# Kernel optimization log

Hardware: AMD Instinct MI355X
Metric: run time of the kernel (lower is better)

## Reference

```python
import jax, jax.numpy as jnp
import numpy as np

N_NODES = 100000
N_EDGES = 1600000
N_FEAT = 128
HIDDEN = 128
N_CLASSES = 10
N_GRAPHS = 512


def setup_inputs() -> dict:
    key = jax.random.key(0)
    ks = jax.random.split(key, 20)

    def lin(k, fan_in, fan_out, bias=True):
        kw, kb = jax.random.split(k)
        s = 1.0 / np.sqrt(fan_in)
        W = jax.random.uniform(kw, (fan_in, fan_out), jnp.float32, -s, s)
        if bias:
            b = jax.random.uniform(kb, (fan_out,), jnp.float32, -s, s)
            return W, b
        return W

    x = jax.random.normal(ks[0], (N_NODES, N_FEAT), jnp.float32)
    edge_index = jax.random.randint(ks[1], (2, N_EDGES), 0, N_NODES)
    batch = jnp.sort(jax.random.randint(ks[2], (N_NODES,), 0, N_GRAPHS))

    w1l, b1 = lin(ks[3], N_FEAT, HIDDEN)
    w1r = lin(ks[4], N_FEAT, HIDDEN, bias=False)
    w2l, b2 = lin(ks[5], HIDDEN, HIDDEN)
    w2r = lin(ks[6], HIDDEN, HIDDEN, bias=False)
    w3l, b3 = lin(ks[7], HIDDEN, HIDDEN)
    w3r = lin(ks[8], HIDDEN, HIDDEN, bias=False)
    gate_w, gate_b = lin(ks[9], HIDDEN, 1)
    lin1_w, lin1_b = lin(ks[10], HIDDEN, HIDDEN)
    lin2_w, lin2_b = lin(ks[11], HIDDEN, N_CLASSES)

    return dict(x=x, edge_index=edge_index, batch=batch,
                w1l=w1l, b1=b1, w1r=w1r,
                w2l=w2l, b2=b2, w2r=w2r,
                w3l=w3l, b3=b3, w3r=w3r,
                gate_w=gate_w, gate_b=gate_b,
                lin1_w=lin1_w, lin1_b=lin1_b,
                lin2_w=lin2_w, lin2_b=lin2_b)


def _sage_conv(x, src, dst, Wl, bl, Wr, n_nodes):
    # PyG SAGEConv(mean): out = lin_l(mean_{j in N(i)} x_j) + lin_r(x_i)
    msg_sum = jax.ops.segment_sum(x[src], dst, num_segments=n_nodes)
    cnt = jax.ops.segment_sum(jnp.ones((src.shape[0], 1), x.dtype), dst,
                              num_segments=n_nodes)
    mean = msg_sum / jnp.maximum(cnt, 1.0)
    return mean @ Wl + bl + x @ Wr


def reference(x, edge_index, batch,
              w1l, b1, w1r, w2l, b2, w2r, w3l, b3, w3r,
              gate_w, gate_b, lin1_w, lin1_b, lin2_w, lin2_b):
    n = x.shape[0]
    src, dst = edge_index[0], edge_index[1]

    h = jax.nn.relu(_sage_conv(x, src, dst, w1l, b1, w1r, n))
    h = jax.nn.relu(_sage_conv(h, src, dst, w2l, b2, w2r, n))
    h = jax.nn.relu(_sage_conv(h, src, dst, w3l, b3, w3r, n))

    # AttentionalAggregation: scatter-softmax of gate over graph segments
    gate = h @ gate_w + gate_b                                  # [N, 1]
    m = jax.ops.segment_max(gate, batch, num_segments=N_GRAPHS)  # [G, 1]
    e = jnp.exp(gate - m[batch])
    s = jax.ops.segment_sum(e, batch, num_segments=N_GRAPHS)     # [G, 1]
    alpha = e / s[batch]
    pooled = jax.ops.segment_sum(alpha * h, batch, num_segments=N_GRAPHS)  # [G, H]

    out = jax.nn.relu(pooled @ lin1_w + lin1_b)
    # dropout is identity in eval mode
    out = out @ lin2_w + lin2_b
    return jax.nn.log_softmax(out, axis=-1)
```

## Files before the change

kernel.cpp:

```cpp
#include <hip/hip_runtime.h>
#include <stdint.h>

#define N_NODES 100000
#define N_EDGES 1600000
#define NF 128
#define NG 512
#define NC 10

#define NBUCK ((N_NODES + 255) / 256)
#define EPB 8192

#define BSTRIDE 264

#define CVT_B 6250
#define BT_B 384
#define BOUNDS_B 3

typedef short short8 __attribute__((ext_vector_type(8)));
typedef float f32x4 __attribute__((ext_vector_type(4)));

__device__ __forceinline__ unsigned short f2b(float f) {
    unsigned u = __float_as_uint(f);
    u += 0x7fffu + ((u >> 16) & 1u);
    return (unsigned short)(u >> 16);
}
__device__ __forceinline__ float lo16(unsigned v) { return __uint_as_float(v << 16); }
__device__ __forceinline__ float hi16(unsigned v) { return __uint_as_float(v & 0xffff0000u); }

__global__ __launch_bounds__(256) void bucket_count(const int* __restrict__ dst, int* __restrict__ bcount) {
    __shared__ int h[NBUCK];
    for (int i = threadIdx.x; i < NBUCK; i += 256) h[i] = 0;
    __syncthreads();
    const int base = blockIdx.x * EPB;
    const int lim = min(base + EPB, N_EDGES);
    for (int i = base + threadIdx.x; i < lim; i += 256) atomicAdd(&h[dst[i] >> 8], 1);
    __syncthreads();
    for (int i = threadIdx.x; i < NBUCK; i += 256)
        if (h[i]) atomicAdd(&bcount[i], h[i]);
}

__global__ __launch_bounds__(512) void bucket_scan(const int* __restrict__ bcount, int* __restrict__ bbase,
                                                   int* __restrict__ gcursor, int* __restrict__ rowptr) {
    __shared__ int sh[512];
    const int t = threadIdx.x;
    int v = (t < NBUCK) ? bcount[t] : 0;
    sh[t] = v;
    __syncthreads();
    for (int off = 1; off < 512; off <<= 1) {
        int u = (t >= off) ? sh[t - off] : 0;
        __syncthreads();
        sh[t] += u;
        __syncthreads();
    }
    if (t < NBUCK) {
        int e = sh[t] - v;
        bbase[t] = e;
        gcursor[t] = e;
    }
    if (t == NBUCK - 1) bbase[NBUCK] = sh[t];
    if (t == 0) rowptr[N_NODES] = N_EDGES;
}

__global__ __launch_bounds__(256) void bucket_scatter(const int* __restrict__ src, const int* __restrict__ dst,
                                                      int* __restrict__ gcursor, unsigned* __restrict__ brec) {
    __shared__ int h[NBUCK];
    for (int i = threadIdx.x; i < NBUCK; i += 256) h[i] = 0;
    __syncthreads();
    const int base = blockIdx.x * EPB;
    const int lim = min(base + EPB, N_EDGES);
    for (int i = base + threadIdx.x; i < lim; i += 256) atomicAdd(&h[dst[i] >> 8], 1);
    __syncthreads();
    for (int i = threadIdx.x; i < NBUCK; i += 256) {
        int c = h[i];
        if (c) h[i] = atomicAdd(&gcursor[i], c);
    }
    __syncthreads();
    for (int i = base + threadIdx.x; i < lim; i += 256) {
        int d = dst[i];
        int pos = atomicAdd(&h[d >> 8], 1);
        brec[pos] = ((unsigned)(d & 255) << 17) | (unsigned)src[i];
    }
}

__global__ __launch_bounds__(256) void bucket_fill(const unsigned* __restrict__ brec, const int* __restrict__ bbase,
                                                   int* __restrict__ rowptr, int* __restrict__ eidx) {
    __shared__ int nh[256];
    __shared__ int sc[256];
    const int b = blockIdx.x, t = threadIdx.x;
    const int beg = bbase[b], end = bbase[b + 1];
    nh[t] = 0;
    __syncthreads();
    for (int i = beg + t; i < end; i += 256) atomicAdd(&nh[brec[i] >> 17], 1);
    __syncthreads();
    int cnt = nh[t];
    sc[t] = cnt;
    __syncthreads();
    for (int off = 1; off < 256; off <<= 1) {
        int u = (t >= off) ? sc[t - off] : 0;
        __syncthreads();
        sc[t] += u;
        __syncthreads();
    }
    int excl = sc[t] - cnt;
    int node = b * 256 + t;
    if (node < N_NODES) rowptr[node] = beg + excl;
    nh[t] = beg + excl;
    __syncthreads();
    for (int i = beg + t; i < end; i += 256) {
        unsigned r = brec[i];
        int pos = atomicAdd(&nh[r >> 17], 1);
        eidx[pos] = (int)(r & 0x1FFFFu);
    }
}

__global__ __launch_bounds__(256) void prep_kernel(const float* __restrict__ x, unsigned short* __restrict__ xb,
                                                   const float* __restrict__ w1l, const float* __restrict__ w1r,
                                                   const float* __restrict__ w2l, const float* __restrict__ w2r,
                                                   const float* __restrict__ w3l, const float* __restrict__ w3r,
                                                   unsigned short* __restrict__ Bt,
                                                   const int* __restrict__ batch, int* __restrict__ gstart) {
    const int b = blockIdx.x, t = threadIdx.x;
    if (b < CVT_B) {
        int i = b * 256 + t;
        const float4* ip = (const float4*)x;
        float4 a = ip[2 * i], c = ip[2 * i + 1];
        uint4 o;
        o.x = (unsigned)f2b(a.x) | ((unsigned)f2b(a.y) << 16);
        o.y = (unsigned)f2b(a.z) | ((unsigned)f2b(a.w) << 16);
        o.z = (unsigned)f2b(c.x) | ((unsigned)f2b(c.y) << 16);
        o.w = (unsigned)f2b(c.z) | ((unsigned)f2b(c.w) << 16);
        ((uint4*)xb)[i] = o;
    } else if (b < CVT_B + BT_B) {
        int i = (b - CVT_B) * 256 + t;
        int layer = i / (128 * 256);
        int r = i % (128 * 256);
        int n = r / 256, k = r % 256;
        const float* wl = (layer == 0) ? w1l : (layer == 1) ? w2l : w3l;
        const float* wr = (layer == 0) ? w1r : (layer == 1) ? w2r : w3r;
        float v = (k < 128) ? wl[k * 128 + n] : wr[(k - 128) * 128 + n];
        Bt[i] = f2b(v);
    } else {
        int g = (b - CVT_B - BT_B) * 256 + t;
        if (g > NG) return;
        int lo = 0, hi = N_NODES;
        while (lo < hi) {
            int mid = (lo + hi) >> 1;
            if (batch[mid] < g) lo = mid + 1; else hi = mid;
        }
        gstart[g] = lo;
    }
}

__global__ __launch_bounds__(256) void agg_kernel(const unsigned short* __restrict__ F,
                                                  const int* __restrict__ rowptr,
                                                  const int* __restrict__ eidx,
                                                  unsigned short* __restrict__ M) {
    int node = blockIdx.x * 4 + (threadIdx.x >> 6);
    if (node >= N_NODES) return;
    const int lane = threadIdx.x & 63;
    const int quad = lane >> 4, ql = lane & 15;
    const int beg = rowptr[node], end = rowptr[node + 1];
    const uint4* F4 = (const uint4*)F;

    float a0 = 0.f, a1 = 0.f, a2 = 0.f, a3 = 0.f, a4 = 0.f, a5 = 0.f, a6 = 0.f, a7 = 0.f;
    int t = beg + quad;
    for (; t + 12 < end; t += 16) {
        int r0 = eidx[t];
        int r1 = eidx[t + 4];
        int r2 = eidx[t + 8];
        int r3 = eidx[t + 12];
        uint4 v0 = F4[(size_t)r0 * 16 + ql];
        uint4 v1 = F4[(size_t)r1 * 16 + ql];
        uint4 v2 = F4[(size_t)r2 * 16 + ql];
        uint4 v3 = F4[(size_t)r3 * 16 + ql];
        a0 += lo16(v0.x) + lo16(v1.x) + lo16(v2.x) + lo16(v3.x);
        a1 += hi16(v0.x) + hi16(v1.x) + hi16(v2.x) + hi16(v3.x);
        a2 += lo16(v0.y) + lo16(v1.y) + lo16(v2.y) + lo16(v3.y);
        a3 += hi16(v0.y) + hi16(v1.y) + hi16(v2.y) + hi16(v3.y);
        a4 += lo16(v0.z) + lo16(v1.z) + lo16(v2.z) + lo16(v3.z);
        a5 += hi16(v0.z) + hi16(v1.z) + hi16(v2.z) + hi16(v3.z);
        a6 += lo16(v0.w) + lo16(v1.w) + lo16(v2.w) + lo16(v3.w);
        a7 += hi16(v0.w) + hi16(v1.w) + hi16(v2.w) + hi16(v3.w);
    }
    for (; t < end; t += 4) {
        uint4 v0 = F4[(size_t)eidx[t] * 16 + ql];
        a0 += lo16(v0.x); a1 += hi16(v0.x);
        a2 += lo16(v0.y); a3 += hi16(v0.y);
        a4 += lo16(v0.z); a5 += hi16(v0.z);
        a6 += lo16(v0.w); a7 += hi16(v0.w);
    }
    a0 += __shfl_xor(a0, 16); a0 += __shfl_xor(a0, 32);
    a1 += __shfl_xor(a1, 16); a1 += __shfl_xor(a1, 32);
    a2 += __shfl_xor(a2, 16); a2 += __shfl_xor(a2, 32);
    a3 += __shfl_xor(a3, 16); a3 += __shfl_xor(a3, 32);
    a4 += __shfl_xor(a4, 16); a4 += __shfl_xor(a4, 32);
    a5 += __shfl_xor(a5, 16); a5 += __shfl_xor(a5, 32);
    a6 += __shfl_xor(a6, 16); a6 += __shfl_xor(a6, 32);
    a7 += __shfl_xor(a7, 16); a7 += __shfl_xor(a7, 32);

    if (quad == 0) {
        float inv = 1.0f / (float)max(end - beg, 1);
        uint4 o;
        o.x = (unsigned)f2b(a0 * inv) | ((unsigned)f2b(a1 * inv) << 16);
        o.y = (unsigned)f2b(a2 * inv) | ((unsigned)f2b(a3 * inv) << 16);
        o.z = (unsigned)f2b(a4 * inv) | ((unsigned)f2b(a5 * inv) << 16);
        o.w = (unsigned)f2b(a6 * inv) | ((unsigned)f2b(a7 * inv) << 16);
        ((uint4*)M)[(size_t)node * 16 + ql] = o;
    }
}

__global__ __launch_bounds__(256, 2) void gemm_kernel(const unsigned short* __restrict__ Am,
                                                      const unsigned short* __restrict__ Ax,
                                                      const unsigned short* __restrict__ Bt,
                                                      const float* __restrict__ bias,
                                                      unsigned short* __restrict__ Out,
                                                      const float* __restrict__ gatew,
                                                      const float* __restrict__ gateb,
                                                      float* __restrict__ gate) {
    const int t = threadIdx.x;
    const int wave = t >> 6, lane = t & 63;
    const int lrow = lane & 15, quad = lane >> 4;
    const int row0 = blockIdx.x * 64 + wave * 16;

    __shared__ __attribute__((aligned(16))) unsigned short Bs[128 * BSTRIDE];

#pragma unroll
    for (int i = 0; i < 16; ++i) {
        int u = t + i * 256;
        int r = u >> 5, seg = u & 31;
        *(uint4*)(Bs + r * BSTRIDE + seg * 8) = *(const uint4*)(Bt + r * 256 + seg * 8);
    }
    __syncthreads();

    int arow = row0 + lrow;
    if (arow > N_NODES - 1) arow = N_NODES - 1;

    f32x4 acc[8];
#pragma unroll
    for (int nt = 0; nt < 8; ++nt) acc[nt] = (f32x4){0.f, 0.f, 0.f, 0.f};

#pragma unroll
    for (int c = 0; c < 8; ++c) {
        const unsigned short* Aarr = (c < 4) ? Am : Ax;
        const int kb = (c & 3) * 32 + quad * 8;
        short8 af = *(const short8*)(Aarr + (size_t)arow * 128 + kb);
        const int kf = c * 32 + quad * 8;
#pragma unroll
        for (int nt = 0; nt < 8; ++nt) {
            short8 bf = *(const short8*)(Bs + (nt * 16 + lrow) * BSTRIDE + kf);
            acc[nt] = __builtin_amdgcn_mfma_f32_16x16x32_bf16(af, bf, acc[nt], 0, 0, 0);
        }
    }

    float gpart[4] = {0.f, 0.f, 0.f, 0.f};
#pragma unroll
    for (int nt = 0; nt < 8; ++nt) {
        int col = nt * 16 + lrow;
        float bc = bias[col];
        float gw = gatew ? gatew[col] : 0.f;
#pragma unroll
        for (int r = 0; r < 4; ++r) {
            int row = row0 + quad * 4 + r;
            if (row < N_NODES) {
                float v = fmaxf(acc[nt][r] + bc, 0.f);
                Out[(size_t)row * 128 + col] = f2b(v);
                gpart[r] += v * gw;
            }
        }
    }
    if (gatew) {
#pragma unroll
        for (int r = 0; r < 4; ++r) {
            gpart[r] += __shfl_xor(gpart[r], 1);
            gpart[r] += __shfl_xor(gpart[r], 2);
            gpart[r] += __shfl_xor(gpart[r], 4);
            gpart[r] += __shfl_xor(gpart[r], 8);
        }
        if (lrow == 0) {
            float gb = gateb[0];
#pragma unroll
            for (int r = 0; r < 4; ++r) {
                int row = row0 + quad * 4 + r;
                if (row < N_NODES) gate[row] = gpart[r] + gb;
            }
        }
    }
}

__global__ __launch_bounds__(256) void pool_mlp_kernel(const unsigned short* __restrict__ h,
                                                       const float* __restrict__ gate,
                                                       const int* __restrict__ gstart,
                                                       const float* __restrict__ l1w,
                                                       const float* __restrict__ l1b,
                                                       const float* __restrict__ l2w,
                                                       const float* __restrict__ l2b,
                                                       float* __restrict__ out) {
    int wv = threadIdx.x >> 6;
    int g = blockIdx.x * 4 + wv;
    int lane = threadIdx.x & 63;
    __shared__ float pooled_s[4][128];
    __shared__ float hid_s[4][128];
    if (g >= NG) return;

    int beg = gstart[g], end = gstart[g + 1];

    float m = -INFINITY;
    for (int i = beg + lane; i < end; i += 64) m = fmaxf(m, gate[i]);
#pragma unroll
    for (int o = 32; o; o >>= 1) m = fmaxf(m, __shfl_xor(m, o));
    float s = 0.f;
    for (int i = beg + lane; i < end; i += 64) s += expf(gate[i] - m);
#pragma unroll
    for (int o = 32; o; o >>= 1) s += __shfl_xor(s, o);
    float invs = (s > 0.f) ? 1.0f / s : 0.f;

    float ax = 0.f, ay = 0.f;
    const unsigned* hb = (const unsigned*)h;
    int i = beg;
    for (; i + 2 <= end; i += 2) {
        float w0 = expf(gate[i] - m) * invs;
        float w1 = expf(gate[i + 1] - m) * invs;
        unsigned v0 = hb[(size_t)i * 64 + lane];
        unsigned v1 = hb[(size_t)(i + 1) * 64 + lane];
        ax += w0 * lo16(v0) + w1 * lo16(v1);
        ay += w0 * hi16(v0) + w1 * hi16(v1);
    }
    for (; i < end; ++i) {
        float w = expf(gate[i] - m) * invs;
        unsigned v = hb[(size_t)i * 64 + lane];
        ax += w * lo16(v);
        ay += w * hi16(v);
    }
    pooled_s[wv][2 * lane] = ax;
    pooled_s[wv][2 * lane + 1] = ay;

    float h0 = l1b[lane], h1 = l1b[lane + 64];
    for (int k = 0; k < 128; ++k) {
        float pv = pooled_s[wv][k];
        h0 += pv * l1w[k * 128 + lane];
        h1 += pv * l1w[k * 128 + lane + 64];
    }
    hid_s[wv][lane] = fmaxf(h0, 0.f);
    hid_s[wv][lane + 64] = fmaxf(h1, 0.f);

    float o10 = 0.f;
    if (lane < NC) {
        o10 = l2b[lane];
        for (int k = 0; k < 128; ++k) o10 += hid_s[wv][k] * l2w[k * NC + lane];
    }
    float mm = -INFINITY;
#pragma unroll
    for (int j = 0; j < NC; ++j) mm = fmaxf(mm, __shfl(o10, j));
    float ss = 0.f;
#pragma unroll
    for (int j = 0; j < NC; ++j) ss += expf(__shfl(o10, j) - mm);
    float lse = mm + logf(ss);
    if (lane < NC) out[g * NC + lane] = o10 - lse;
}

extern "C" void kernel_launch(void* const* d_in, const int* in_sizes, int n_in,
                              void* d_out, int out_size, void* d_ws, size_t ws_size,
                              hipStream_t stream) {
    const float* x   = (const float*)d_in[0];
    const int* ei    = (const int*)d_in[1];
    const int* batch = (const int*)d_in[2];
    const float* w1l = (const float*)d_in[3];
    const float* b1  = (const float*)d_in[4];
    const float* w1r = (const float*)d_in[5];
    const float* w2l = (const float*)d_in[6];
    const float* b2  = (const float*)d_in[7];
    const float* w2r = (const float*)d_in[8];
    const float* w3l = (const float*)d_in[9];
    const float* b3  = (const float*)d_in[10];
    const float* w3r = (const float*)d_in[11];
    const float* gw  = (const float*)d_in[12];
    const float* gb  = (const float*)d_in[13];
    const float* l1w = (const float*)d_in[14];
    const float* l1b = (const float*)d_in[15];
    const float* l2w = (const float*)d_in[16];
    const float* l2b = (const float*)d_in[17];
    float* out = (float*)d_out;

    const int* src = ei;
    const int* dst = ei + N_EDGES;

    char* base = (char*)d_ws;
    size_t off = 0;
    auto carve = [&](size_t bytes) -> void* {
        void* r = base + off;
        off = (off + bytes + 255) & ~(size_t)255;
        return r;
    };
    int* rowptr         = (int*)carve((size_t)(N_NODES + 1) * 4);
    int* eidx           = (int*)carve((size_t)N_EDGES * 4);
    unsigned short* Bt  = (unsigned short*)carve((size_t)3 * 128 * 256 * 2);
    unsigned short* xb  = (unsigned short*)carve((size_t)N_NODES * NF * 2);
    unsigned short* mn  = (unsigned short*)carve((size_t)N_NODES * NF * 2);
    unsigned short* hA  = (unsigned short*)carve((size_t)N_NODES * NF * 2);
    unsigned short* hB  = (unsigned short*)carve((size_t)N_NODES * NF * 2);
    float* gate         = (float*)carve((size_t)N_NODES * 4);
    int* gstart         = (int*)carve(513 * 4);
    int* bcount         = (int*)carve((NBUCK + 1) * 4);
    int* bbase          = (int*)carve((NBUCK + 1) * 4);
    int* gcursor        = (int*)carve((NBUCK + 1) * 4);
    unsigned* brec      = (unsigned*)mn;

    hipMemsetAsync(bcount, 0, (size_t)NBUCK * 4, stream);

    const int BUCK_B = (N_EDGES + EPB - 1) / EPB;
    bucket_count<<<BUCK_B, 256, 0, stream>>>(dst, bcount);
    bucket_scan<<<1, 512, 0, stream>>>(bcount, bbase, gcursor, rowptr);
    bucket_scatter<<<BUCK_B, 256, 0, stream>>>(src, dst, gcursor, brec);
    bucket_fill<<<NBUCK, 256, 0, stream>>>(brec, bbase, rowptr, eidx);

    prep_kernel<<<CVT_B + BT_B + BOUNDS_B, 256, 0, stream>>>(x, xb, w1l, w1r, w2l, w2r, w3l, w3r,
                                                             Bt, batch, gstart);

    const int AGG_B = (N_NODES + 3) / 4;
    const int GEMM_B = (N_NODES + 63) / 64;

    agg_kernel<<<AGG_B, 256, 0, stream>>>(xb, rowptr, eidx, mn);
    gemm_kernel<<<GEMM_B, 256, 0, stream>>>(mn, xb, Bt, b1, hA, nullptr, nullptr, nullptr);
    agg_kernel<<<AGG_B, 256, 0, stream>>>(hA, rowptr, eidx, mn);
    gemm_kernel<<<GEMM_B, 256, 0, stream>>>(mn, hA, Bt + 32768, b2, hB, nullptr, nullptr, nullptr);
    agg_kernel<<<AGG_B, 256, 0, stream>>>(hB, rowptr, eidx, mn);
    gemm_kernel<<<GEMM_B, 256, 0, stream>>>(mn, hB, Bt + 65536, b3, hA, gw, gb, gate);

    pool_mlp_kernel<<<(NG + 3) / 4, 256, 0, stream>>>(hA, gate, gstart, l1w, l1b, l2w, l2b, out);
}
```

Before: 521.7 us.

## Fold bucket counting into prep, persistent GEMM grid, per-graph pool blocks

Merges the edge bucket-count kernel into the prep kernel as extra blocks, removing one launch, and halves edges-per-block for counting and scatter. The GEMM becomes a persistent 512-block grid that stages B in shared memory once per block and loops over row tiles, instead of reloading the weights in each of roughly 1563 blocks. The pool/MLP kernel now uses one 64-thread block per graph instead of four waves per block. These cut launch count and repeated weight staging, at the cost of less GEMM parallelism and more global atomics from the smaller count blocks.

```diff
diff --git a/kernel.cpp b/kernel.cpp
--- a/kernel.cpp
+++ b/kernel.cpp
@@ -8,13 +8,16 @@
 #define NC 10
 
 #define NBUCK ((N_NODES + 255) / 256)
-#define EPB 8192
+#define EPB 4096
 
 #define BSTRIDE 264
+#define GEMM_GRID 512
+#define N_TILES ((N_NODES + 63) / 64)
 
 #define CVT_B 6250
 #define BT_B 384
 #define BOUNDS_B 3
+#define COUNT_B ((N_EDGES + EPB - 1) / EPB)
 
 typedef short short8 __attribute__((ext_vector_type(8)));
 typedef float f32x4 __attribute__((ext_vector_type(4)));
@@ -26,99 +29,14 @@
 }
 __device__ __forceinline__ float lo16(unsigned v) { return __uint_as_float(v << 16); }
 __device__ __forceinline__ float hi16(unsigned v) { return __uint_as_float(v & 0xffff0000u); }
-
-__global__ __launch_bounds__(256) void bucket_count(const int* __restrict__ dst, int* __restrict__ bcount) {
-    __shared__ int h[NBUCK];
-    for (int i = threadIdx.x; i < NBUCK; i += 256) h[i] = 0;
-    __syncthreads();
-    const int base = blockIdx.x * EPB;
-    const int lim = min(base + EPB, N_EDGES);
-    for (int i = base + threadIdx.x; i < lim; i += 256) atomicAdd(&h[dst[i] >> 8], 1);
-    __syncthreads();
-    for (int i = threadIdx.x; i < NBUCK; i += 256)
-        if (h[i]) atomicAdd(&bcount[i], h[i]);
-}
-
-__global__ __launch_bounds__(512) void bucket_scan(const int* __restrict__ bcount, int* __restrict__ bbase,
-                                                   int* __restrict__ gcursor, int* __restrict__ rowptr) {
-    __shared__ int sh[512];
-    const int t = threadIdx.x;
-    int v = (t < NBUCK) ? bcount[t] : 0;
-    sh[t] = v;
-    __syncthreads();
-    for (int off = 1; off < 512; off <<= 1) {
-        int u = (t >= off) ? sh[t - off] : 0;
-        __syncthreads();
-        sh[t] += u;
-        __syncthreads();
-    }
-    if (t < NBUCK) {
-        int e = sh[t] - v;
-        bbase[t] = e;
-        gcursor[t] = e;
-    }
-    if (t == NBUCK - 1) bbase[NBUCK] = sh[t];
-    if (t == 0) rowptr[N_NODES] = N_EDGES;
-}
-
-__global__ __launch_bounds__(256) void bucket_scatter(const int* __restrict__ src, const int* __restrict__ dst,
-                                                      int* __restrict__ gcursor, unsigned* __restrict__ brec) {
-    __shared__ int h[NBUCK];
-    for (int i = threadIdx.x; i < NBUCK; i += 256) h[i] = 0;
-    __syncthreads();
-    const int base = blockIdx.x * EPB;
-    const int lim = min(base + EPB, N_EDGES);
-    for (int i = base + threadIdx.x; i < lim; i += 256) atomicAdd(&h[dst[i] >> 8], 1);
-    __syncthreads();
-    for (int i = threadIdx.x; i < NBUCK; i += 256) {
-        int c = h[i];
-        if (c) h[i] = atomicAdd(&gcursor[i], c);
-    }
-    __syncthreads();
-    for (int i = base + threadIdx.x; i < lim; i += 256) {
-        int d = dst[i];
-        int pos = atomicAdd(&h[d >> 8], 1);
-        brec[pos] = ((unsigned)(d & 255) << 17) | (unsigned)src[i];
-    }
-}
-
-__global__ __launch_bounds__(256) void bucket_fill(const unsigned* __restrict__ brec, const int* __restrict__ bbase,
-                                                   int* __restrict__ rowptr, int* __restrict__ eidx) {
-    __shared__ int nh[256];
-    __shared__ int sc[256];
-    const int b = blockIdx.x, t = threadIdx.x;
-    const int beg = bbase[b], end = bbase[b + 1];
-    nh[t] = 0;
-    __syncthreads();
-    for (int i = beg + t; i < end; i += 256) atomicAdd(&nh[brec[i] >> 17], 1);
-    __syncthreads();
-    int cnt = nh[t];
-    sc[t] = cnt;
-    __syncthreads();
-    for (int off = 1; off < 256; off <<= 1) {
-        int u = (t >= off) ? sc[t - off] : 0;
-        __syncthreads();
-        sc[t] += u;
-        __syncthreads();
-    }
-    int excl = sc[t] - cnt;
-    int node = b * 256 + t;
-    if (node < N_NODES) rowptr[node] = beg + excl;
-    nh[t] = beg + excl;
-    __syncthreads();
-    for (int i = beg + t; i < end; i += 256) {
-        unsigned r = brec[i];
-        int pos = atomicAdd(&nh[r >> 17], 1);
-        eidx[pos] = (int)(r & 0x1FFFFu);
-    }
-}
 
 __global__ __launch_bounds__(256) void prep_kernel(const float* __restrict__ x, unsigned short* __restrict__ xb,
                                                    const float* __restrict__ w1l, const float* __restrict__ w1r,
                                                    const float* __restrict__ w2l, const float* __restrict__ w2r,
                                                    const float* __restrict__ w3l, const float* __restrict__ w3r,
                                                    unsigned short* __restrict__ Bt,
-                                                   const int* __restrict__ batch, int* __restrict__ gstart) {
+                                                   const int* __restrict__ batch, int* __restrict__ gstart,
+                                                   const int* __restrict__ dst, int* __restrict__ bcount) {
     const int b = blockIdx.x, t = threadIdx.x;
     if (b < CVT_B) {
         int i = b * 256 + t;
@@ -139,7 +57,7 @@
         const float* wr = (layer == 0) ? w1r : (layer == 1) ? w2r : w3r;
         float v = (k < 128) ? wl[k * 128 + n] : wr[(k - 128) * 128 + n];
         Bt[i] = f2b(v);
-    } else {
+    } else if (b < CVT_B + BT_B + BOUNDS_B) {
         int g = (b - CVT_B - BT_B) * 256 + t;
         if (g > NG) return;
         int lo = 0, hi = N_NODES;
@@ -148,6 +66,90 @@
             if (batch[mid] < g) lo = mid + 1; else hi = mid;
         }
         gstart[g] = lo;
+    } else {
+        __shared__ int h[NBUCK];
+        for (int i = t; i < NBUCK; i += 256) h[i] = 0;
+        __syncthreads();
+        const int base = (b - CVT_B - BT_B - BOUNDS_B) * EPB;
+        const int lim = min(base + EPB, N_EDGES);
+        for (int i = base + t; i < lim; i += 256) atomicAdd(&h[dst[i] >> 8], 1);
+        __syncthreads();
+        for (int i = t; i < NBUCK; i += 256)
+            if (h[i]) atomicAdd(&bcount[i], h[i]);
+    }
+}
+
+__global__ __launch_bounds__(512) void bucket_scan(const int* __restrict__ bcount, int* __restrict__ bbase,
+                                                   int* __restrict__ gcursor, int* __restrict__ rowptr) {
+    __shared__ int sh[512];
+    const int t = threadIdx.x;
+    int v = (t < NBUCK) ? bcount[t] : 0;
+    sh[t] = v;
+    __syncthreads();
+    for (int off = 1; off < 512; off <<= 1) {
+        int u = (t >= off) ? sh[t - off] : 0;
+        __syncthreads();
+        sh[t] += u;
+        __syncthreads();
+    }
+    if (t < NBUCK) {
+        int e = sh[t] - v;
+        bbase[t] = e;
+        gcursor[t] = e;
+    }
+    if (t == NBUCK - 1) bbase[NBUCK] = sh[t];
+    if (t == 0) rowptr[N_NODES] = N_EDGES;
+}
+
+__global__ __launch_bounds__(256) void bucket_scatter(const int* __restrict__ src, const int* __restrict__ dst,
+                                                      int* __restrict__ gcursor, unsigned* __restrict__ brec) {
+    __shared__ int h[NBUCK];
+    for (int i = threadIdx.x; i < NBUCK; i += 256) h[i] = 0;
+    __syncthreads();
+    const int base = blockIdx.x * EPB;
+    const int lim = min(base + EPB, N_EDGES);
+    for (int i = base + threadIdx.x; i < lim; i += 256) atomicAdd(&h[dst[i] >> 8], 1);
+    __syncthreads();
+    for (int i = threadIdx.x; i < NBUCK; i += 256) {
+        int c = h[i];
+        if (c) h[i] = atomicAdd(&gcursor[i], c);
+    }
+    __syncthreads();
+    for (int i = base + threadIdx.x; i < lim; i += 256) {
+        int d = dst[i];
+        int pos = atomicAdd(&h[d >> 8], 1);
+        brec[pos] = ((unsigned)(d & 255) << 17) | (unsigned)src[i];
+    }
+}
+
+__global__ __launch_bounds__(256) void bucket_fill(const unsigned* __restrict__ brec, const int* __restrict__ bbase,
+                                                   int* __restrict__ rowptr, int* __restrict__ eidx) {
+    __shared__ int nh[256];
+    __shared__ int sc[256];
+    const int b = blockIdx.x, t = threadIdx.x;
+    const int beg = bbase[b], end = bbase[b + 1];
+    nh[t] = 0;
+    __syncthreads();
+    for (int i = beg + t; i < end; i += 256) atomicAdd(&nh[brec[i] >> 17], 1);
+    __syncthreads();
+    int cnt = nh[t];
+    sc[t] = cnt;
+    __syncthreads();
+    for (int off = 1; off < 256; off <<= 1) {
+        int u = (t >= off) ? sc[t - off] : 0;
+        __syncthreads();
+        sc[t] += u;
+        __syncthreads();
+    }
+    int excl = sc[t] - cnt;
+    int node = b * 256 + t;
+    if (node < N_NODES) rowptr[node] = beg + excl;
+    nh[t] = beg + excl;
+    __syncthreads();
+    for (int i = beg + t; i < end; i += 256) {
+        unsigned r = brec[i];
+        int pos = atomicAdd(&nh[r >> 17], 1);
+        eidx[pos] = (int)(r & 0x1FFFFu);
     }
 }
 
@@ -220,7 +222,6 @@
     const int t = threadIdx.x;
     const int wave = t >> 6, lane = t & 63;
     const int lrow = lane & 15, quad = lane >> 4;
-    const int row0 = blockIdx.x * 64 + wave * 16;
 
     __shared__ __attribute__((aligned(16))) unsigned short Bs[128 * BSTRIDE];
 
@@ -232,75 +233,74 @@
     }
     __syncthreads();
 
-    int arow = row0 + lrow;
-    if (arow > N_NODES - 1) arow = N_NODES - 1;
-
-    f32x4 acc[8];
-#pragma unroll
-    for (int nt = 0; nt < 8; ++nt) acc[nt] = (f32x4){0.f, 0.f, 0.f, 0.f};
-
-#pragma unroll
-    for (int c = 0; c < 8; ++c) {
-        const unsigned short* Aarr = (c < 4) ? Am : Ax;
-        const int kb = (c & 3) * 32 + quad * 8;
-        short8 af = *(const short8*)(Aarr + (size_t)arow * 128 + kb);
-        const int kf = c * 32 + quad * 8;
-#pragma unroll
-        for (int nt = 0; nt < 8; ++nt) {
-            short8 bf = *(const short8*)(Bs + (nt * 16 + lrow) * BSTRIDE + kf);
-            acc[nt] = __builtin_amdgcn_mfma_f32_16x16x32_bf16(af, bf, acc[nt], 0, 0, 0);
-        }
-    }
-
-    float gpart[4] = {0.f, 0.f, 0.f, 0.f};
-#pragma unroll
-    for (int nt = 0; nt < 8; ++nt) {
-        int col = nt * 16 + lrow;
-        float bc = bias[col];
-        float gw = gatew ? gatew[col] : 0.f;
-#pragma unroll
-        for (int r = 0; r < 4; ++r) {
-            int row = row0 + quad * 4 + r;
-            if (row < N_NODES) {
-                float v = fmaxf(acc[nt][r] + bc, 0.f);
-                Out[(size_t)row * 128 + col] = f2b(v);
-                gpart[r] += v * gw;
+    for (int tile = blockIdx.x; tile < N_TILES; tile += GEMM_GRID) {
+        const int row0 = tile * 64 + wave * 16;
+        int arow = row0 + lrow;
+        if (arow > N_NODES - 1) arow = N_NODES - 1;
+
+        f32x4 acc[8];
+#pragma unroll
+        for (int nt = 0; nt < 8; ++nt) acc[nt] = (f32x4){0.f, 0.f, 0.f, 0.f};
+
+#pragma unroll
+        for (int c = 0; c < 8; ++c) {
+            const unsigned short* Aarr = (c < 4) ? Am : Ax;
+            const int kb = (c & 3) * 32 + quad * 8;
+            short8 af = *(const short8*)(Aarr + (size_t)arow * 128 + kb);
+            const int kf = c * 32 + quad * 8;
+#pragma unroll
+            for (int nt = 0; nt < 8; ++nt) {
+                short8 bf = *(const short8*)(Bs + (nt * 16 + lrow) * BSTRIDE + kf);
+                acc[nt] = __builtin_amdgcn_mfma_f32_16x16x32_bf16(af, bf, acc[nt], 0, 0, 0);
             }
         }
-    }
-    if (gatew) {
-#pragma unroll
-        for (int r = 0; r < 4; ++r) {
-            gpart[r] += __shfl_xor(gpart[r], 1);
-            gpart[r] += __shfl_xor(gpart[r], 2);
-            gpart[r] += __shfl_xor(gpart[r], 4);
-            gpart[r] += __shfl_xor(gpart[r], 8);
-        }
-        if (lrow == 0) {
-            float gb = gateb[0];
+
+        float gpart[4] = {0.f, 0.f, 0.f, 0.f};
+#pragma unroll
+        for (int nt = 0; nt < 8; ++nt) {
+            int col = nt * 16 + lrow;
+            float bc = bias[col];
+            float gw = gatew ? gatew[col] : 0.f;
 #pragma unroll
             for (int r = 0; r < 4; ++r) {
                 int row = row0 + quad * 4 + r;
-                if (row < N_NODES) gate[row] = gpart[r] + gb;
+                if (row < N_NODES) {
+                    float v = fmaxf(acc[nt][r] + bc, 0.f);
+                    Out[(size_t)row * 128 + col] = f2b(v);
+                    gpart[r] += v * gw;
+                }
             }
         }
-    }
-}
-
-__global__ __launch_bounds__(256) void pool_mlp_kernel(const unsigned short* __restrict__ h,
-                                                       const float* __restrict__ gate,
-                                                       const int* __restrict__ gstart,
-                                                       const float* __restrict__ l1w,
-                                                       const float* __restrict__ l1b,
-                                                       const float* __restrict__ l2w,
-                                                       const float* __restrict__ l2b,
-                                                       float* __restrict__ out) {
-    int wv = threadIdx.x >> 6;
-    int g = blockIdx.x * 4 + wv;
-    int lane = threadIdx.x & 63;
-    __shared__ float pooled_s[4][128];
-    __shared__ float hid_s[4][128];
-    if (g >= NG) return;
+        if (gatew) {
+            float gb = gateb[0];
+#pragma unroll
+            for (int r = 0; r < 4; ++r) {
+                float g = gpart[r];
+                g += __shfl_xor(g, 1);
+                g += __shfl_xor(g, 2);
+                g += __shfl_xor(g, 4);
+                g += __shfl_xor(g, 8);
+                if (lrow == 0) {
+                    int row = row0 + quad * 4 + r;
+                    if (row < N_NODES) gate[row] = g + gb;
+                }
+            }
+        }
+    }
+}
+
+__global__ __launch_bounds__(64) void pool_mlp_kernel(const unsigned short* __restrict__ h,
+                                                      const float* __restrict__ gate,
+                                                      const int* __restrict__ gstart,
+                                                      const float* __restrict__ l1w,
+                                                      const float* __restrict__ l1b,
+                                                      const float* __restrict__ l2w,
+                                                      const float* __restrict__ l2b,
+                                                      float* __restrict__ out) {
+    int g = blockIdx.x;
+    int lane = threadIdx.x;
+    __shared__ float pooled_s[128];
+    __shared__ float hid_s[128];
 
     int beg = gstart[g], end = gstart[g + 1];
 
@@ -331,22 +331,24 @@
         ax += w * lo16(v);
         ay += w * hi16(v);
     }
-    pooled_s[wv][2 * lane] = ax;
-    pooled_s[wv][2 * lane + 1] = ay;
+    pooled_s[2 * lane] = ax;
+    pooled_s[2 * lane + 1] = ay;
+    __syncthreads();
 
     float h0 = l1b[lane], h1 = l1b[lane + 64];
     for (int k = 0; k < 128; ++k) {
-        float pv = pooled_s[wv][k];
+        float pv = pooled_s[k];
         h0 += pv * l1w[k * 128 + lane];
         h1 += pv * l1w[k * 128 + lane + 64];
     }
-    hid_s[wv][lane] = fmaxf(h0, 0.f);
-    hid_s[wv][lane + 64] = fmaxf(h1, 0.f);
+    hid_s[lane] = fmaxf(h0, 0.f);
+    hid_s[lane + 64] = fmaxf(h1, 0.f);
+    __syncthreads();
 
     float o10 = 0.f;
     if (lane < NC) {
         o10 = l2b[lane];
-        for (int k = 0; k < 128; ++k) o10 += hid_s[wv][k] * l2w[k * NC + lane];
+        for (int k = 0; k < 128; ++k) o10 += hid_s[k] * l2w[k * NC + lane];
     }
     float mm = -INFINITY;
 #pragma unroll
@@ -407,24 +409,21 @@
 
     hipMemsetAsync(bcount, 0, (size_t)NBUCK * 4, stream);
 
-    const int BUCK_B = (N_EDGES + EPB - 1) / EPB;
-    bucket_count<<<BUCK_B, 256, 0, stream>>>(dst, bcount);
+    prep_kernel<<<CVT_B + BT_B + BOUNDS_B + COUNT_B, 256, 0, stream>>>(
+        x, xb, w1l, w1r, w2l, w2r, w3l, w3r, Bt, batch, gstart, dst, bcount);
+
     bucket_scan<<<1, 512, 0, stream>>>(bcount, bbase, gcursor, rowptr);
-    bucket_scatter<<<BUCK_B, 256, 0, stream>>>(src, dst, gcursor, brec);
+    bucket_scatter<<<COUNT_B, 256, 0, stream>>>(src, dst, gcursor, brec);
     bucket_fill<<<NBUCK, 256, 0, stream>>>(brec, bbase, rowptr, eidx);
 
-    prep_kernel<<<CVT_B + BT_B + BOUNDS_B, 256, 0, stream>>>(x, xb, w1l, w1r, w2l, w2r, w3l, w3r,
-                                                             Bt, batch, gstart);
-
     const int AGG_B = (N_NODES + 3) / 4;
-    const int GEMM_B = (N_NODES + 63) / 64;
 
     agg_kernel<<<AGG_B, 256, 0, stream>>>(xb, rowptr, eidx, mn);
-    gemm_kernel<<<GEMM_B, 256, 0, stream>>>(mn, xb, Bt, b1, hA, nullptr, nullptr, nullptr);
+    gemm_kernel<<<GEMM_GRID, 256, 0, stream>>>(mn, xb, Bt, b1, hA, nullptr, nullptr, nullptr);
     agg_kernel<<<AGG_B, 256, 0, stream>>>(hA, rowptr, eidx, mn);
-    gemm_kernel<<<GEMM_B, 256, 0, stream>>>(mn, hA, Bt + 32768, b2, hB, nullptr, nullptr, nullptr);
+    gemm_kernel<<<GEMM_GRID, 256, 0, stream>>>(mn, hA, Bt + 32768, b2, hB, nullptr, nullptr, nullptr);
     agg_kernel<<<AGG_B, 256, 0, stream>>>(hB, rowptr, eidx, mn);
-    gemm_kernel<<<GEMM_B, 256, 0, stream>>>(mn, hB, Bt + 65536, b3, hA, gw, gb, gate);
-
-    pool_mlp_kernel<<<(NG + 3) / 4, 256, 0, stream>>>(hA, gate, gstart, l1w, l1b, l2w, l2b, out);
-}
+    gemm_kernel<<<GEMM_GRID, 256, 0, stream>>>(mn, hB, Bt + 65536, b3, hA, gw, gb, gate);
+
+    pool_mlp_kernel<<<NG, 64, 0, stream>>>(hA, gate, gstart, l1w, l1b, l2w, l2b, out);
+}
```

Measured after the change: 581.5 us. 1.11x slower.
